# Kernel tuning notes

Hardware: AMD Instinct MI355X
Metric: run time of the kernel (lower is better)

The kernel has to match this reference:

```python
import jax, jax.numpy as jnp
import numpy as np

FP8_E4M3_MAX = 448.0  # torch.float8_e4m3fn max


def _fp8_quant(x, scale):
    # per-tensor static-scale fp8 quantization: clamp(x/scale) -> e4m3 -> back to f32
    q = jnp.clip(x / scale, -FP8_E4M3_MAX, FP8_E4M3_MAX)
    return q.astype(jnp.float8_e4m3fn).astype(jnp.float32)


def setup_inputs() -> dict:
    key = jax.random.key(0)
    k1, k2, k3 = jax.random.split(key, 3)
    M, K, N = 8192, 4096, 11008
    inp = jax.random.normal(k1, (M, K), dtype=jnp.float32)
    # weight is stored pre-quantized (fp8 values held as fp32), already transposed to [K, N]
    w = jax.random.normal(k2, (K, N), dtype=jnp.float32) * 0.02
    weight_scale = jnp.float32(0.01)
    qweight = _fp8_quant(w, weight_scale)
    qbias = jax.random.normal(k3, (N,), dtype=jnp.float32) * 0.01
    input_scale = jnp.float32(0.05)
    return {
        "input": inp,
        "qweight": qweight,
        "qbias": qbias,
        "weight_scale": weight_scale,
        "input_scale": input_scale,
    }


def reference(input, qweight, qbias, weight_scale, input_scale) -> jnp.ndarray:
    # scaled_fp8_quant with a provided static scale: x_scale == input_scale
    qinput = _fp8_quant(input, input_scale)  # [M, K], fp8 values in f32
    # cutlass_scaled_mm / _scaled_mm: (qinput * x_scale) @ (qweight * weight_scale) + bias
    out = jnp.einsum("mk,kn->mn", qinput, qweight) * (input_scale * weight_scale)
    out = out + qbias[None, :]
    return out.astype(input.dtype)
```

## Files before the change

kernel.cpp:

```cpp
#include <hip/hip_runtime.h>

typedef float v16f __attribute__((ext_vector_type(16)));
typedef int   v8i  __attribute__((ext_vector_type(8)));
typedef int   v4i  __attribute__((ext_vector_type(4)));

#define BM 128
#define BN 128
#define BK 64

__device__ __forceinline__ unsigned int pack4_fp8(float a, float b, float c, float d) {
    unsigned int v = __builtin_amdgcn_cvt_pk_fp8_f32(a, b, 0, false);
    v = __builtin_amdgcn_cvt_pk_fp8_f32(c, d, v, true);
    return v;
}

__global__ __launch_bounds__(256) void quant_x_kernel(
    const float* __restrict__ X, const float* __restrict__ sp,
    unsigned int* __restrict__ Q)
{
    const long i = (long)blockIdx.x * 256 + threadIdx.x;
    const float s = sp[0];
    const float4 v = ((const float4*)X)[i];
    const float a = fminf(fmaxf(v.x / s, -448.f), 448.f);
    const float b = fminf(fmaxf(v.y / s, -448.f), 448.f);
    const float c = fminf(fmaxf(v.z / s, -448.f), 448.f);
    const float d = fminf(fmaxf(v.w / s, -448.f), 448.f);
    Q[i] = pack4_fp8(a, b, c, d);
}

__global__ __launch_bounds__(256) void quant_wT_kernel(
    const float* __restrict__ Wf, unsigned char* __restrict__ Wq, int K, int N)
{
    const int k0 = blockIdx.x * 64;
    const int n0 = blockIdx.y * 64;
    const int t  = threadIdx.x;
    const int n  = t >> 2;
    const int kc = (t & 3) * 16;
    const float* src = Wf + (long)(k0 + kc) * N + n0 + n;
    unsigned int o[4];
#pragma unroll
    for (int j = 0; j < 4; ++j) {
        const float x0 = src[(long)(4 * j + 0) * N];
        const float x1 = src[(long)(4 * j + 1) * N];
        const float x2 = src[(long)(4 * j + 2) * N];
        const float x3 = src[(long)(4 * j + 3) * N];
        o[j] = pack4_fp8(x0, x1, x2, x3);
    }
    uint4 q; q.x = o[0]; q.y = o[1]; q.z = o[2]; q.w = o[3];
    *(uint4*)(Wq + (long)(n0 + n) * K + k0 + kc) = q;
}

__device__ __forceinline__ void async_copy16(const void* g, void* l) {
    __builtin_amdgcn_global_load_lds(
        (const __attribute__((address_space(1))) unsigned int*)g,
        (__attribute__((address_space(3))) unsigned int*)l,
        16, 0, 0);
}

__device__ __forceinline__ v8i ld_frag(const unsigned char* base, int row, int c0) {
    const int sw = (row >> 1) & 3;
    const v4i lo = *(const v4i*)(base + row * 64 + (((c0    ) ^ sw) << 4));
    const v4i hi = *(const v4i*)(base + row * 64 + (((c0 + 1) ^ sw) << 4));
    v8i f;
    f[0] = lo[0]; f[1] = lo[1]; f[2] = lo[2]; f[3] = lo[3];
    f[4] = hi[0]; f[5] = hi[1]; f[6] = hi[2]; f[7] = hi[3];
    return f;
}

__global__ __launch_bounds__(256) void fp8_gemm_kernel(
    const unsigned char* __restrict__ A8,
    const unsigned char* __restrict__ B8,
    const float* __restrict__ bias,
    const float* __restrict__ ws_p, const float* __restrict__ is_p,
    float* __restrict__ C, int M, int N, int K)
{
    __shared__ unsigned char AsB[BM * BK];
    __shared__ unsigned char BsB[BN * BK];

    const int tid = threadIdx.x;
    const int l   = tid & 63;
    const int w   = tid >> 6;
    const int wr  = w >> 1, wc = w & 1;
    const int lrow = l & 31;
    const int c0   = (l >> 5) * 2;

    const long m0 = (long)blockIdx.y * BM;
    const long n0 = (long)blockIdx.x * BN;

    const int srow = tid >> 2;
    const int sch  = (tid & 3) ^ ((tid >> 3) & 3);
    const unsigned char* aG = A8 + (m0 + srow) * (long)K + sch * 16;
    const unsigned char* bG = B8 + (n0 + srow) * (long)K + sch * 16;
    const long rowStep = (long)64 * K;

    v16f acc[2][2];
#pragma unroll
    for (int i = 0; i < 2; ++i)
#pragma unroll
        for (int j = 0; j < 2; ++j)
#pragma unroll
            for (int e = 0; e < 16; ++e)
                acc[i][j][e] = 0.f;

    for (int kt = 0; kt < K; kt += BK) {
        async_copy16(aG + kt,           AsB + tid * 16);
        async_copy16(aG + kt + rowStep, AsB + 4096 + tid * 16);
        async_copy16(bG + kt,           BsB + tid * 16);
        async_copy16(bG + kt + rowStep, BsB + 4096 + tid * 16);
        __syncthreads();

        v8i a[2], b[2];
#pragma unroll
        for (int mt = 0; mt < 2; ++mt)
            a[mt] = ld_frag(AsB, wr * 64 + mt * 32 + lrow, c0);
#pragma unroll
        for (int nt = 0; nt < 2; ++nt)
            b[nt] = ld_frag(BsB, wc * 64 + nt * 32 + lrow, c0);

#pragma unroll
        for (int mt = 0; mt < 2; ++mt)
#pragma unroll
            for (int nt = 0; nt < 2; ++nt)
                acc[mt][nt] = __builtin_amdgcn_mfma_scale_f32_32x32x64_f8f6f4(
                    a[mt], b[nt], acc[mt][nt],
                    0 , 0 ,
                    0, 0x7F7F7F7Fu ,
                    0, 0x7F7F7F7Fu );
        __syncthreads();
    }

    const float s = is_p[0] * ws_p[0];
#pragma unroll
    for (int mt = 0; mt < 2; ++mt)
#pragma unroll
        for (int nt = 0; nt < 2; ++nt) {
            const long cc = n0 + wc * 64 + nt * 32 + lrow;
            const float bv = bias[cc];
            float* dst = C + (m0 + wr * 64 + mt * 32 + (l >> 5) * 4) * (long)N + cc;
#pragma unroll
            for (int g = 0; g < 4; ++g)
#pragma unroll
                for (int r = 0; r < 4; ++r)
                    dst[(long)(g * 8 + r) * N] = acc[mt][nt][g * 4 + r] * s + bv;
        }
}

extern "C" void kernel_launch(void* const* d_in, const int* in_sizes, int n_in,
                              void* d_out, int out_size, void* d_ws, size_t ws_size,
                              hipStream_t stream)
{
    const float* X    = (const float*)d_in[0];
    const float* Wf   = (const float*)d_in[1];
    const float* bias = (const float*)d_in[2];
    const float* wsc  = (const float*)d_in[3];
    const float* isc  = (const float*)d_in[4];
    float* out = (float*)d_out;

    const int N = in_sizes[2];
    const int K = in_sizes[1] / N;
    const int M = in_sizes[0] / K;

    unsigned char* A8 = (unsigned char*)d_ws;
    unsigned char* B8 = A8 + (size_t)M * K;

    quant_x_kernel<<<dim3((unsigned)((long)M * K / 4 / 256)), 256, 0, stream>>>(
        X, isc, (unsigned int*)A8);

    quant_wT_kernel<<<dim3(K / 64, N / 64), 256, 0, stream>>>(Wf, B8, K, N);

    fp8_gemm_kernel<<<dim3(N / BN, M / BM), 256, 0, stream>>>(
        A8, B8, bias, wsc, isc, out, M, N, K);
}
```

Before: 1.109 ms.

## Enlarge GEMM tiles to 256x256 and add a triple-buffered async LDS pipeline

The fp8 GEMM tile grows from 128x128 to 256x256 and runs with 512 threads. Each wave now computes a 128x64 sub-tile, so every LDS fragment load feeds more MFMAs. Global-to-LDS loads become a 3-slot ring that prefetches two K-steps ahead, gated by explicit vmcnt waits and raw barriers, so memory latency overlaps compute. It also remaps workgroup IDs in groups of eight to improve L2 locality, raises wave priority around the MFMA block, and precomputes the swizzled LDS offsets. In exchange, 96KB of LDS per block and more accumulator registers limit occupancy.

```diff
diff --git a/kernel.cpp b/kernel.cpp
--- a/kernel.cpp
+++ b/kernel.cpp
@@ -4,9 +4,11 @@
 typedef int   v8i  __attribute__((ext_vector_type(8)));
 typedef int   v4i  __attribute__((ext_vector_type(4)));
 
-#define BM 128
-#define BN 128
-#define BK 64
+#define BM 256
+#define BN 256
+#define BKB 64
+#define NBUF 3
+#define TILE_AB 16384
 
 __device__ __forceinline__ unsigned int pack4_fp8(float a, float b, float c, float d) {
     unsigned int v = __builtin_amdgcn_cvt_pk_fp8_f32(a, b, 0, false);
@@ -57,86 +59,142 @@
         16, 0, 0);
 }
 
-__device__ __forceinline__ v8i ld_frag(const unsigned char* base, int row, int c0) {
-    const int sw = (row >> 1) & 3;
-    const v4i lo = *(const v4i*)(base + row * 64 + (((c0    ) ^ sw) << 4));
-    const v4i hi = *(const v4i*)(base + row * 64 + (((c0 + 1) ^ sw) << 4));
-    v8i f;
-    f[0] = lo[0]; f[1] = lo[1]; f[2] = lo[2]; f[3] = lo[3];
-    f[4] = hi[0]; f[5] = hi[1]; f[6] = hi[2]; f[7] = hi[3];
-    return f;
-}
-
-__global__ __launch_bounds__(256) void fp8_gemm_kernel(
+__global__ __launch_bounds__(512, 2) void fp8_gemm_kernel(
     const unsigned char* __restrict__ A8,
     const unsigned char* __restrict__ B8,
     const float* __restrict__ bias,
     const float* __restrict__ ws_p, const float* __restrict__ is_p,
     float* __restrict__ C, int M, int N, int K)
 {
-    __shared__ unsigned char AsB[BM * BK];
-    __shared__ unsigned char BsB[BN * BK];
+    __shared__ unsigned char AsB[NBUF * TILE_AB];
+    __shared__ unsigned char BsB[NBUF * TILE_AB];
 
     const int tid = threadIdx.x;
     const int l   = tid & 63;
     const int w   = tid >> 6;
-    const int wr  = w >> 1, wc = w & 1;
+    const int wr  = w >> 2, wc = w & 3;
     const int lrow = l & 31;
     const int c0   = (l >> 5) * 2;
 
-    const long m0 = (long)blockIdx.y * BM;
-    const long n0 = (long)blockIdx.x * BN;
+    int bx = blockIdx.x, by = blockIdx.y;
+    {
+        const int gx = gridDim.x, nwg = gridDim.x * gridDim.y;
+        if ((nwg & 7) == 0) {
+            const int id  = by * gx + bx;
+            const int cpx = nwg >> 3;
+            const int swz = (id & 7) * cpx + (id >> 3);
+            bx = swz % gx;
+            by = swz / gx;
+        }
+    }
+    const long m0 = (long)by * BM;
+    const long n0 = (long)bx * BN;
 
     const int srow = tid >> 2;
     const int sch  = (tid & 3) ^ ((tid >> 3) & 3);
     const unsigned char* aG = A8 + (m0 + srow) * (long)K + sch * 16;
     const unsigned char* bG = B8 + (n0 + srow) * (long)K + sch * 16;
-    const long rowStep = (long)64 * K;
-
-    v16f acc[2][2];
-#pragma unroll
-    for (int i = 0; i < 2; ++i)
+    const long rowStep = (long)128 * K;
+
+    int offA0[4], offA1[4], offB0[2], offB1[2];
+#pragma unroll
+    for (int mt = 0; mt < 4; ++mt) {
+        const int r  = wr * 128 + mt * 32 + lrow;
+        const int sw = (r >> 1) & 3;
+        offA0[mt] = r * 64 + (((c0    ) ^ sw) << 4);
+        offA1[mt] = r * 64 + (((c0 + 1) ^ sw) << 4);
+    }
+#pragma unroll
+    for (int nt = 0; nt < 2; ++nt) {
+        const int r  = wc * 64 + nt * 32 + lrow;
+        const int sw = (r >> 1) & 3;
+        offB0[nt] = r * 64 + (((c0    ) ^ sw) << 4);
+        offB1[nt] = r * 64 + (((c0 + 1) ^ sw) << 4);
+    }
+
+    v16f acc[4][2];
+#pragma unroll
+    for (int i = 0; i < 4; ++i)
 #pragma unroll
         for (int j = 0; j < 2; ++j)
 #pragma unroll
             for (int e = 0; e < 16; ++e)
                 acc[i][j][e] = 0.f;
 
-    for (int kt = 0; kt < K; kt += BK) {
-        async_copy16(aG + kt,           AsB + tid * 16);
-        async_copy16(aG + kt + rowStep, AsB + 4096 + tid * 16);
-        async_copy16(bG + kt,           BsB + tid * 16);
-        async_copy16(bG + kt + rowStep, BsB + 4096 + tid * 16);
-        __syncthreads();
-
-        v8i a[2], b[2];
-#pragma unroll
-        for (int mt = 0; mt < 2; ++mt)
-            a[mt] = ld_frag(AsB, wr * 64 + mt * 32 + lrow, c0);
-#pragma unroll
-        for (int nt = 0; nt < 2; ++nt)
-            b[nt] = ld_frag(BsB, wc * 64 + nt * 32 + lrow, c0);
-
-#pragma unroll
-        for (int mt = 0; mt < 2; ++mt)
+    const int NT = K / BKB;
+
+    auto stage = [&](int ktB, int slot) {
+        const unsigned char* ag = aG + ktB;
+        const unsigned char* bg = bG + ktB;
+        unsigned char* al = AsB + slot * TILE_AB + tid * 16;
+        unsigned char* bl = BsB + slot * TILE_AB + tid * 16;
+        async_copy16(ag,           al);
+        async_copy16(ag + rowStep, al + 8192);
+        async_copy16(bg,           bl);
+        async_copy16(bg + rowStep, bl + 8192);
+    };
+
+    stage(0, 0);
+    stage(BKB, 1);
+
+    int sl_c = 0, sl_p = 2;
+    for (int t = 0; t < NT; ++t) {
+        if (t + 2 < NT) {
+            stage((t + 2) * BKB, sl_p);
+            asm volatile("s_waitcnt vmcnt(8)" ::: "memory");
+        } else if (t + 2 == NT) {
+            asm volatile("s_waitcnt vmcnt(4)" ::: "memory");
+        } else {
+            asm volatile("s_waitcnt vmcnt(0)" ::: "memory");
+        }
+        __builtin_amdgcn_s_barrier();
+        __builtin_amdgcn_sched_barrier(0);
+
+        const unsigned char* Ab = AsB + sl_c * TILE_AB;
+        const unsigned char* Bb = BsB + sl_c * TILE_AB;
+        v8i a[4], b[2];
+#pragma unroll
+        for (int mt = 0; mt < 4; ++mt) {
+            const v4i lo = *(const v4i*)(Ab + offA0[mt]);
+            const v4i hi = *(const v4i*)(Ab + offA1[mt]);
+            v8i f; f[0]=lo[0]; f[1]=lo[1]; f[2]=lo[2]; f[3]=lo[3];
+                   f[4]=hi[0]; f[5]=hi[1]; f[6]=hi[2]; f[7]=hi[3];
+            a[mt] = f;
+        }
+#pragma unroll
+        for (int nt = 0; nt < 2; ++nt) {
+            const v4i lo = *(const v4i*)(Bb + offB0[nt]);
+            const v4i hi = *(const v4i*)(Bb + offB1[nt]);
+            v8i f; f[0]=lo[0]; f[1]=lo[1]; f[2]=lo[2]; f[3]=lo[3];
+                   f[4]=hi[0]; f[5]=hi[1]; f[6]=hi[2]; f[7]=hi[3];
+            b[nt] = f;
+        }
+
+        __builtin_amdgcn_s_setprio(1);
+#pragma unroll
+        for (int mt = 0; mt < 4; ++mt)
 #pragma unroll
             for (int nt = 0; nt < 2; ++nt)
                 acc[mt][nt] = __builtin_amdgcn_mfma_scale_f32_32x32x64_f8f6f4(
                     a[mt], b[nt], acc[mt][nt],
                     0 , 0 ,
-                    0, 0x7F7F7F7Fu ,
-                    0, 0x7F7F7F7Fu );
-        __syncthreads();
+                    0, 0x7F7F7F7Fu, 0, 0x7F7F7F7Fu );
+        __builtin_amdgcn_s_setprio(0);
+
+        __builtin_amdgcn_sched_barrier(0);
+        __builtin_amdgcn_s_barrier();
+        sl_c = (sl_c == 2) ? 0 : sl_c + 1;
+        sl_p = (sl_p == 2) ? 0 : sl_p + 1;
     }
 
     const float s = is_p[0] * ws_p[0];
 #pragma unroll
-    for (int mt = 0; mt < 2; ++mt)
+    for (int mt = 0; mt < 4; ++mt)
 #pragma unroll
         for (int nt = 0; nt < 2; ++nt) {
             const long cc = n0 + wc * 64 + nt * 32 + lrow;
             const float bv = bias[cc];
-            float* dst = C + (m0 + wr * 64 + mt * 32 + (l >> 5) * 4) * (long)N + cc;
+            float* dst = C + (m0 + wr * 128 + mt * 32 + (l >> 5) * 4) * (long)N + cc;
 #pragma unroll
             for (int g = 0; g < 4; ++g)
 #pragma unroll
@@ -168,6 +226,6 @@
 
     quant_wT_kernel<<<dim3(K / 64, N / 64), 256, 0, stream>>>(Wf, B8, K, N);
 
-    fp8_gemm_kernel<<<dim3(N / BN, M / BM), 256, 0, stream>>>(
+    fp8_gemm_kernel<<<dim3(N / BN, M / BM), 512, 0, stream>>>(
         A8, B8, bias, wsc, isc, out, M, N, K);
 }
```

Measured after the change: 1.047 ms. 1.06x faster.

## Rework FP8 GEMM into 256x256 double-buffered pipelined tiles with block swizzle

Applied to the files above, without the earlier changes.

The GEMM moves from 128x128 tiles with 4 waves to 256x256 tiles with 8 waves and two LDS buffers. Async global-to-LDS loads for the next K slices are interleaved with eight MFMA phases under explicit barriers, waitcnts and raised wave priority, so memory latency hides behind compute and each tile reuses more data. Workgroup IDs are remapped to improve L2 locality. The weight-quantize kernel now transposes through shared memory for coalesced reads. The cost is 128KB of LDS per block, which allows only one block per CU, and a fragile hand-written wait schedule.

```diff
diff --git a/kernel.cpp b/kernel.cpp
--- a/kernel.cpp
+++ b/kernel.cpp
@@ -4,9 +4,11 @@
 typedef int   v8i  __attribute__((ext_vector_type(8)));
 typedef int   v4i  __attribute__((ext_vector_type(4)));
 
-#define BM 128
-#define BN 128
-#define BK 64
+#define BM 256
+#define BN 256
+#define SC1 0x7F7F7FFu + 0x7F000000u
+
+static constexpr unsigned SCONE = 0x7F7F7F7Fu;
 
 __device__ __forceinline__ unsigned int pack4_fp8(float a, float b, float c, float d) {
     unsigned int v = __builtin_amdgcn_cvt_pk_fp8_f32(a, b, 0, false);
@@ -31,23 +33,28 @@
 __global__ __launch_bounds__(256) void quant_wT_kernel(
     const float* __restrict__ Wf, unsigned char* __restrict__ Wq, int K, int N)
 {
+    __shared__ float T[64][68];
+    const int tid = threadIdx.x;
     const int k0 = blockIdx.x * 64;
     const int n0 = blockIdx.y * 64;
-    const int t  = threadIdx.x;
-    const int n  = t >> 2;
-    const int kc = (t & 3) * 16;
-    const float* src = Wf + (long)(k0 + kc) * N + n0 + n;
+    const int rr = tid >> 4;
+    const int cc = (tid & 15) * 4;
+#pragma unroll
+    for (int j = 0; j < 4; ++j) {
+        const int r = j * 16 + rr;
+        const float4 v = *(const float4*)(Wf + (long)(k0 + r) * N + n0 + cc);
+        T[r][cc + 0] = v.x; T[r][cc + 1] = v.y; T[r][cc + 2] = v.z; T[r][cc + 3] = v.w;
+    }
+    __syncthreads();
+    const int n  = tid >> 2;
+    const int kc = (tid & 3) * 16;
     unsigned int o[4];
 #pragma unroll
-    for (int j = 0; j < 4; ++j) {
-        const float x0 = src[(long)(4 * j + 0) * N];
-        const float x1 = src[(long)(4 * j + 1) * N];
-        const float x2 = src[(long)(4 * j + 2) * N];
-        const float x3 = src[(long)(4 * j + 3) * N];
-        o[j] = pack4_fp8(x0, x1, x2, x3);
-    }
-    uint4 q; q.x = o[0]; q.y = o[1]; q.z = o[2]; q.w = o[3];
-    *(uint4*)(Wq + (long)(n0 + n) * K + k0 + kc) = q;
+    for (int q = 0; q < 4; ++q)
+        o[q] = pack4_fp8(T[kc + q*4 + 0][n], T[kc + q*4 + 1][n],
+                         T[kc + q*4 + 2][n], T[kc + q*4 + 3][n]);
+    uint4 out; out.x = o[0]; out.y = o[1]; out.z = o[2]; out.w = o[3];
+    *(uint4*)(Wq + (long)(n0 + n) * K + k0 + kc) = out;
 }
 
 __device__ __forceinline__ void async_copy16(const void* g, void* l) {
@@ -57,86 +64,151 @@
         16, 0, 0);
 }
 
-__device__ __forceinline__ v8i ld_frag(const unsigned char* base, int row, int c0) {
-    const int sw = (row >> 1) & 3;
-    const v4i lo = *(const v4i*)(base + row * 64 + (((c0    ) ^ sw) << 4));
-    const v4i hi = *(const v4i*)(base + row * 64 + (((c0 + 1) ^ sw) << 4));
-    v8i f;
-    f[0] = lo[0]; f[1] = lo[1]; f[2] = lo[2]; f[3] = lo[3];
-    f[4] = hi[0]; f[5] = hi[1]; f[6] = hi[2]; f[7] = hi[3];
+__device__ __forceinline__ v8i ld32(const unsigned char* p, int o0, int o1) {
+    const v4i lo = *(const v4i*)(p + o0);
+    const v4i hi = *(const v4i*)(p + o1);
+    v8i f; f[0]=lo[0]; f[1]=lo[1]; f[2]=lo[2]; f[3]=lo[3];
+           f[4]=hi[0]; f[5]=hi[1]; f[6]=hi[2]; f[7]=hi[3];
     return f;
 }
 
-__global__ __launch_bounds__(256) void fp8_gemm_kernel(
+__global__ __launch_bounds__(512, 2) void fp8_gemm_kernel(
     const unsigned char* __restrict__ A8,
     const unsigned char* __restrict__ B8,
     const float* __restrict__ bias,
     const float* __restrict__ ws_p, const float* __restrict__ is_p,
     float* __restrict__ C, int M, int N, int K)
 {
-    __shared__ unsigned char AsB[BM * BK];
-    __shared__ unsigned char BsB[BN * BK];
+    __shared__ unsigned char AsB[2 * 32768];
+    __shared__ unsigned char BsB[2 * 32768];
 
     const int tid = threadIdx.x;
     const int l   = tid & 63;
     const int w   = tid >> 6;
-    const int wr  = w >> 1, wc = w & 1;
+    const int wr  = w >> 2, wc = w & 3;
     const int lrow = l & 31;
-    const int c0   = (l >> 5) * 2;
-
-    const long m0 = (long)blockIdx.y * BM;
-    const long n0 = (long)blockIdx.x * BN;
-
-    const int srow = tid >> 2;
-    const int sch  = (tid & 3) ^ ((tid >> 3) & 3);
-    const unsigned char* aG = A8 + (m0 + srow) * (long)K + sch * 16;
-    const unsigned char* bG = B8 + (n0 + srow) * (long)K + sch * 16;
-    const long rowStep = (long)64 * K;
-
-    v16f acc[2][2];
-#pragma unroll
-    for (int i = 0; i < 2; ++i)
+    const int h    = l >> 5;
+    const int sw   = lrow & 7;
+
+    int bx = blockIdx.x, by = blockIdx.y;
+    {
+        const int gx = gridDim.x, nwg = gridDim.x * gridDim.y;
+        if ((nwg & 7) == 0) {
+            const int id  = by * gx + bx;
+            const int cpx = nwg >> 3;
+            const int swz = (id & 7) * cpx + (id >> 3);
+            bx = swz % gx;
+            by = swz / gx;
+        }
+    }
+    const long m0 = (long)by * BM;
+    const long n0 = (long)bx * BN;
+
+    const int  chOff = (((tid & 7) ^ ((tid >> 3) & 7)) << 4);
+    const long K64  = (long)64  * K;
+    const long K32  = (long)32  * K;
+    const long K128 = (long)128 * K;
+    const unsigned char* aSrc = A8 + (m0 + (tid >> 3)) * (long)K + chOff;
+    const unsigned char* bSrc = B8 + (n0 + (tid >> 8) * 64 + ((tid >> 3) & 31)) * (long)K + chOff;
+    const int bDst = (tid >> 8) * 8192 + ((tid >> 3) & 31) * 128 + (tid & 7) * 16;
+
+    unsigned char* As0 = AsB;          unsigned char* As1 = AsB + 32768;
+    unsigned char* Bs0 = BsB;          unsigned char* Bs1 = BsB + 32768;
+
+    const int aRdBase = (wr * 128 + lrow) * 128;
+    const int bRdBase = (wc * 64  + lrow) * 128;
+    const int c00 = (((0 + h*2 + 0) ^ sw) << 4);
+    const int c01 = (((0 + h*2 + 1) ^ sw) << 4);
+    const int c10 = (((4 + h*2 + 0) ^ sw) << 4);
+    const int c11 = (((4 + h*2 + 1) ^ sw) << 4);
+
+    v16f acc[4][2];
+#pragma unroll
+    for (int i = 0; i < 4; ++i)
 #pragma unroll
         for (int j = 0; j < 2; ++j)
 #pragma unroll
             for (int e = 0; e < 16; ++e)
                 acc[i][j][e] = 0.f;
 
-    for (int kt = 0; kt < K; kt += BK) {
-        async_copy16(aG + kt,           AsB + tid * 16);
-        async_copy16(aG + kt + rowStep, AsB + 4096 + tid * 16);
-        async_copy16(bG + kt,           BsB + tid * 16);
-        async_copy16(bG + kt + rowStep, BsB + 4096 + tid * 16);
-        __syncthreads();
-
-        v8i a[2], b[2];
-#pragma unroll
-        for (int mt = 0; mt < 2; ++mt)
-            a[mt] = ld_frag(AsB, wr * 64 + mt * 32 + lrow, c0);
-#pragma unroll
-        for (int nt = 0; nt < 2; ++nt)
-            b[nt] = ld_frag(BsB, wc * 64 + nt * 32 + lrow, c0);
-
-#pragma unroll
-        for (int mt = 0; mt < 2; ++mt)
-#pragma unroll
-            for (int nt = 0; nt < 2; ++nt)
-                acc[mt][nt] = __builtin_amdgcn_mfma_scale_f32_32x32x64_f8f6f4(
-                    a[mt], b[nt], acc[mt][nt],
-                    0 , 0 ,
-                    0, 0x7F7F7F7Fu ,
-                    0, 0x7F7F7F7Fu );
-        __syncthreads();
+#define STAGE_A(DSTBASE, QM, TBYTE) do { \
+    const unsigned char* s_ = aSrc + (TBYTE) + (QM) * K64; \
+    async_copy16(s_,        (DSTBASE) + (QM) * 8192 + tid * 16); \
+    async_copy16(s_ + K128, (DSTBASE) + 16384 + (QM) * 8192 + tid * 16); \
+} while (0)
+
+#define STAGE_B(DSTBASE, QN, TBYTE) do { \
+    const unsigned char* s_ = bSrc + (TBYTE) + (QN) * K32; \
+    async_copy16(s_,        (DSTBASE) + (QN) * 4096 + bDst); \
+    async_copy16(s_ + K128, (DSTBASE) + 16384 + (QN) * 4096 + bDst); \
+} while (0)
+
+#define MFMA(AV, BV, D) \
+    D = __builtin_amdgcn_mfma_scale_f32_32x32x64_f8f6f4( \
+        (AV), (BV), (D), 0, 0, 0, SCONE, 0, SCONE)
+
+#define PHASE(ABUF, BBUF, QM, QN, STAGE_CODE, WAIT_CODE) do { \
+    const unsigned char* Ab_ = (ABUF); \
+    const unsigned char* Bb_ = (BBUF); \
+    const v8i a0k0 = ld32(Ab_ + aRdBase + (QM)*8192,        c00, c01); \
+    const v8i a0k1 = ld32(Ab_ + aRdBase + (QM)*8192,        c10, c11); \
+    const v8i a1k0 = ld32(Ab_ + aRdBase + (QM)*8192 + 4096, c00, c01); \
+    const v8i a1k1 = ld32(Ab_ + aRdBase + (QM)*8192 + 4096, c10, c11); \
+    const v8i b0   = ld32(Bb_ + bRdBase + (QN)*4096,        c00, c01); \
+    const v8i b1   = ld32(Bb_ + bRdBase + (QN)*4096,        c10, c11); \
+    STAGE_CODE; \
+    __builtin_amdgcn_s_barrier(); \
+    asm volatile("s_waitcnt lgkmcnt(0)" ::: "memory"); \
+    __builtin_amdgcn_sched_barrier(0); \
+    __builtin_amdgcn_s_setprio(1); \
+    MFMA(a0k0, b0, acc[(QM)*2 + 0][QN]); \
+    MFMA(a1k0, b0, acc[(QM)*2 + 1][QN]); \
+    MFMA(a0k1, b1, acc[(QM)*2 + 0][QN]); \
+    MFMA(a1k1, b1, acc[(QM)*2 + 1][QN]); \
+    __builtin_amdgcn_s_setprio(0); \
+    __builtin_amdgcn_sched_barrier(0); \
+    WAIT_CODE; \
+    __builtin_amdgcn_s_barrier(); \
+    __builtin_amdgcn_sched_barrier(0); \
+} while (0)
+
+    STAGE_A(As0, 0, 0);   STAGE_B(Bs0, 0, 0);
+    STAGE_A(As0, 1, 0);   STAGE_B(Bs0, 1, 0);
+    STAGE_A(As1, 0, 128); STAGE_B(Bs1, 0, 128);
+    asm volatile("s_waitcnt vmcnt(4)" ::: "memory");
+    __builtin_amdgcn_s_barrier();
+
+    const int NIT = K >> 8;
+    for (int it = 0; it < NIT; ++it) {
+        const long tB = (long)it << 8;
+        const bool lst = (it == NIT - 1);
+
+        PHASE(As0, Bs0, 0, 0, { STAGE_A(As1, 1, tB + 128); }, {});
+        PHASE(As0, Bs0, 0, 1, { STAGE_B(Bs1, 1, tB + 128); }, {});
+        PHASE(As0, Bs0, 1, 0, { if (!lst) STAGE_A(As0, 0, tB + 256); }, {});
+        PHASE(As0, Bs0, 1, 1, { if (!lst) STAGE_B(Bs0, 0, tB + 256); },
+              { if (!lst) { asm volatile("s_waitcnt vmcnt(4)" ::: "memory"); }
+                else      { asm volatile("s_waitcnt vmcnt(0)" ::: "memory"); } });
+        PHASE(As1, Bs1, 0, 0, { if (!lst) STAGE_A(As0, 1, tB + 256); }, {});
+        PHASE(As1, Bs1, 0, 1, { if (!lst) STAGE_B(Bs0, 1, tB + 256); }, {});
+        PHASE(As1, Bs1, 1, 0, { if (!lst) STAGE_A(As1, 0, tB + 384); }, {});
+        PHASE(As1, Bs1, 1, 1, { if (!lst) STAGE_B(Bs1, 0, tB + 384); },
+              { if (!lst) { asm volatile("s_waitcnt vmcnt(4)" ::: "memory"); } });
     }
 
+#undef PHASE
+#undef MFMA
+#undef STAGE_A
+#undef STAGE_B
+
     const float s = is_p[0] * ws_p[0];
 #pragma unroll
-    for (int mt = 0; mt < 2; ++mt)
+    for (int mt = 0; mt < 4; ++mt)
 #pragma unroll
         for (int nt = 0; nt < 2; ++nt) {
             const long cc = n0 + wc * 64 + nt * 32 + lrow;
             const float bv = bias[cc];
-            float* dst = C + (m0 + wr * 64 + mt * 32 + (l >> 5) * 4) * (long)N + cc;
+            float* dst = C + (m0 + wr * 128 + mt * 32 + h * 4) * (long)N + cc;
 #pragma unroll
             for (int g = 0; g < 4; ++g)
 #pragma unroll
@@ -168,6 +240,6 @@
 
     quant_wT_kernel<<<dim3(K / 64, N / 64), 256, 0, stream>>>(Wf, B8, K, N);
 
-    fp8_gemm_kernel<<<dim3(N / BN, M / BM), 256, 0, stream>>>(
+    fp8_gemm_kernel<<<dim3(N / BN, M / BM), 512, 0, stream>>>(
         A8, B8, bias, wsc, isc, out, M, N, K);
 }
```

Result: slower. 1.173 ms (+5.8%).
